# Kernel tuning notes

Hardware: AMD Instinct MI355X
Metric: run time of the kernel (lower is better)

The kernel has to match this reference:

```python
import jax, jax.numpy as jnp
import numpy as np

D_MODEL = 1024
NHEAD = 16
HEAD_DIM = D_MODEL // NHEAD
EPS = 1e-8


def setup_inputs() -> dict:
    key = jax.random.key(0)
    ks = jax.random.split(key, 10)
    B, T = 2, 2048
    s = 1.0 / np.sqrt(D_MODEL)
    return {
        "query": jax.random.normal(ks[0], (B, T, D_MODEL), jnp.float32),
        "key": jax.random.normal(ks[1], (B, T, D_MODEL), jnp.float32),
        "value": jax.random.normal(ks[2], (B, T, D_MODEL), jnp.float32),
        "frac": jax.random.uniform(ks[3], (B, T), jnp.float32),
        "Wq": jax.random.normal(ks[4], (D_MODEL, D_MODEL), jnp.float32) * s,
        "bq": jnp.zeros((D_MODEL,), jnp.float32),
        "Wk": jax.random.normal(ks[5], (D_MODEL, D_MODEL), jnp.float32) * s,
        "bk": jnp.zeros((D_MODEL,), jnp.float32),
        "Wv": jax.random.normal(ks[6], (D_MODEL, D_MODEL), jnp.float32) * s,
        "bv": jnp.zeros((D_MODEL,), jnp.float32),
        "attn_bias": jax.random.normal(ks[7], (HEAD_DIM,), jnp.float32) * 0.02,
        "Wo": jax.random.normal(ks[8], (D_MODEL, D_MODEL), jnp.float32) * s,
        "bo": jnpp if False else jnp.zeros((D_MODEL,), jnp.float32),
    }


def reference(query, key, value, frac, Wq, bq, Wk, bk, Wv, bv, attn_bias, Wo, bo):
    B, T, _ = query.shape
    H, Dh = NHEAD, HEAD_DIM
    scale = Dh ** -0.5

    # torch Linear: x @ W.T + b
    Q = (query @ Wq.T + bq).reshape(B, T, H, Dh).transpose(0, 2, 1, 3)  # [B,H,T,Dh]
    K = (key @ Wk.T + bk).reshape(B, T, H, Dh).transpose(0, 2, 1, 3)
    V = (value @ Wv.T + bv).reshape(B, T, H, Dh).transpose(0, 2, 1, 3)

    # factor_ij = (frac_j - frac_i) / (frac_i*frac_j + eps), shape [B,T,T]
    fi = frac[:, :, None]
    fj = frac[:, None, :]
    factor = (fj - fi) / (fi * fj + EPS)

    # sum_d (Q_i*K_j + attn_bias*factor)_d == QK^T + sum(attn_bias)*factor
    bias_sum = jnp.sum(attn_bias)
    logits = jnp.einsum('bhid,bhjd->bhij', Q, K) + bias_sum * factor[:, None, :, :]
    logits = logits * scale

    probs = jax.nn.softmax(logits, axis=-1)  # dropout p=0.0 (eval)
    out = jnp.einsum('bhij,bhjd->bhid', probs, V)  # [B,H,T,Dh]
    out = out.transpose(0, 2, 1, 3).reshape(B, T, H * Dh)
    return out @ Wo.T + bo
```

## Files before the change

kernel.cpp:

```cpp
#include <hip/hip_runtime.h>

typedef short s16x8 __attribute__((ext_vector_type(8)));
typedef float f32x4 __attribute__((ext_vector_type(4)));
typedef unsigned int u32x2 __attribute__((ext_vector_type(2)));
typedef unsigned short u16;
typedef unsigned int u32;

#define D_MODEL 1024
#define NHEAD   16
#define HD      64
#define TSEQ    2048
#define NB      2
#define MROWS   4096

#define LOG2E 1.4426950408889634f
#define QSCALE (0.125f * LOG2E)

__device__ __forceinline__ u16 f2bf(float f) {
  unsigned u = __builtin_bit_cast(unsigned, f);
  u += 0x7fffu + ((u >> 16) & 1u);
  return (u16)(u >> 16);
}

__device__ __forceinline__ u32 cvtpk(float lo, float hi) {
  u32 r;
  asm("v_cvt_pk_bf16_f32 %0, %1, %2" : "=v"(r) : "v"(lo), "v"(hi));
  return r;
}

__device__ __forceinline__ float exp2fast(float x) {
#if __has_builtin(__builtin_amdgcn_exp2f)
  return __builtin_amdgcn_exp2f(x);
#else
  return exp2f(x);
#endif
}

__device__ __forceinline__ float rcpfast(float x) {
#if __has_builtin(__builtin_amdgcn_rcpf)
  return __builtin_amdgcn_rcpf(x);
#else
  return 1.f / x;
#endif
}

__device__ __forceinline__ void gload16(const void* g, void* l) {
  __builtin_amdgcn_global_load_lds((const __attribute__((address_space(1))) void*)g,
                                   (__attribute__((address_space(3))) void*)l,
                                   16, 0, 0);
}

__global__ void cvt_all(const float* __restrict__ q, const float* __restrict__ k,
                        const float* __restrict__ v, const float* __restrict__ wq,
                        const float* __restrict__ wk, const float* __restrict__ wv,
                        const float* __restrict__ wo, const float* __restrict__ ab,
                        u16* qb, u16* kb, u16* vb, u16* wqb, u16* wkb, u16* wvb, u16* wob,
                        float* bsum) {
  if (blockIdx.x == 16384) {
    if (threadIdx.x < 64) {
      float s = ab[threadIdx.x];
#pragma unroll
      for (int m = 32; m >= 1; m >>= 1) s += __shfl_xor(s, m);
      if (threadIdx.x == 0) bsum[0] = s * 0.125f * LOG2E;
    }
    return;
  }
  int i = blockIdx.x * 256 + threadIdx.x;
  const float* src; u16* dst; int off;
  if (i < 3 * 1048576) {
    int t = i >> 20; off = i & 1048575;
    src = (t == 0) ? q : (t == 1) ? k : v;
    dst = (t == 0) ? qb : (t == 1) ? kb : vb;
  } else {
    int j = i - 3 * 1048576;
    int t = j >> 18; off = j & 262143;
    src = (t == 0) ? wq : (t == 1) ? wk : (t == 2) ? wv : wo;
    dst = (t == 0) ? wqb : (t == 1) ? wkb : (t == 2) ? wvb : wob;
  }
  float4 x = ((const float4*)src)[off];
  ushort4 o;
  o.x = f2bf(x.x); o.y = f2bf(x.y); o.z = f2bf(x.z); o.w = f2bf(x.w);
  ((ushort4*)dst)[off] = o;
}

template <int BM, int BN, int WN>
__device__ __forceinline__ void gemm_core(const u16* __restrict__ A, const u16* __restrict__ Bt,
                                          const float* __restrict__ bias, void* __restrict__ out,
                                          float oscale, int mode, u16* lds) {
  constexpr int K = 1024, N = 1024;
  constexpr int WM = 4 / WN;
  constexpr int WTM = BM / WM, WTN = BN / WN;
  constexpr int MR = WTM / 16, NR = WTN / 16;
  constexpr int ASZ = BM * 32, BSZ = BN * 32;
  constexpr int AISS = ASZ / 2048, BISS = BSZ / 2048;
  u16* lA = lds;
  u16* lB = lds + 2 * ASZ;

  const int tid = threadIdx.x;
  const int wid = tid >> 6, lane = tid & 63;
  const int l15 = lane & 15, lgp = lane >> 4;
  const int wr = wid / WN, wc = wid % WN;
  const int m0 = blockIdx.y * BM, n0 = blockIdx.x * BN;

  const u16* gA[AISS];
  const u16* gB[BISS];
#pragma unroll
  for (int i = 0; i < AISS; ++i) {
    int tp = i * 256 + tid, row = tp % BM, kc = tp / BM;
    gA[i] = A + (size_t)(m0 + row) * K + kc * 8;
  }
#pragma unroll
  for (int i = 0; i < BISS; ++i) {
    int tp = i * 256 + tid, row = tp % BN, kc = tp / BN;
    gB[i] = Bt + (size_t)(n0 + row) * K + kc * 8;
  }

  f32x4 acc[MR][NR];
#pragma unroll
  for (int m = 0; m < MR; ++m)
#pragma unroll
    for (int n = 0; n < NR; ++n) acc[m][n] = (f32x4){0.f, 0.f, 0.f, 0.f};

  auto stage = [&](int buf, int k0) {
#pragma unroll
    for (int i = 0; i < AISS; ++i)
      gload16(gA[i] + k0, lA + buf * ASZ + (i * 256 + tid) * 8);
#pragma unroll
    for (int i = 0; i < BISS; ++i)
      gload16(gB[i] + k0, lB + buf * BSZ + (i * 256 + tid) * 8);
  };

  int cur = 0;
  stage(0, 0);
  __syncthreads();
  for (int k0 = 0; k0 < K; k0 += 32) {
    if (k0 + 32 < K) stage(cur ^ 1, k0 + 32);
    const u16* a = lA + cur * ASZ;
    const u16* b = lB + cur * BSZ;
    s16x8 af[MR], bf[NR];
#pragma unroll
    for (int m = 0; m < MR; ++m)
      af[m] = *(const s16x8*)(a + lgp * BM * 8 + (wr * WTM + m * 16 + l15) * 8);
#pragma unroll
    for (int n = 0; n < NR; ++n)
      bf[n] = *(const s16x8*)(b + lgp * BN * 8 + (wc * WTN + n * 16 + l15) * 8);
    __builtin_amdgcn_s_setprio(1);
#pragma unroll
    for (int m = 0; m < MR; ++m)
#pragma unroll
      for (int n = 0; n < NR; ++n)
        acc[m][n] = __builtin_amdgcn_mfma_f32_16x16x32_bf16(af[m], bf[n], acc[m][n], 0, 0, 0);
    __builtin_amdgcn_s_setprio(0);
    __syncthreads();
    cur ^= 1;
  }

  float bvv[NR];
#pragma unroll
  for (int n = 0; n < NR; ++n) bvv[n] = bias[n0 + wc * WTN + n * 16 + l15];

#pragma unroll
  for (int m = 0; m < MR; ++m) {
    int rowb = m0 + wr * WTM + m * 16 + lgp * 4;
#pragma unroll
    for (int n = 0; n < NR; ++n) {
      int col = n0 + wc * WTN + n * 16 + l15;
#pragma unroll
      for (int r = 0; r < 4; ++r) {
        int row = rowb + r;
        float vv = (acc[m][n][r] + bvv[n]) * oscale;
        if (mode == 2) {
          ((float*)out)[(size_t)row * N + col] = vv;
        } else {
          int b = row >> 11, t = row & 2047;
          int h = col >> 6, d = col & 63;
          u16 x = f2bf(vv);
          if (mode == 0)
            ((u16*)out)[(((size_t)(b * NHEAD + h) * TSEQ + t) << 6) + d] = x;
          else
            ((u16*)out)[(((size_t)(b * NHEAD + h) * HD + d) << 11) + t] = x;
        }
      }
    }
  }
}

__global__ __launch_bounds__(256) void gemm_qkv(const u16* __restrict__ qb, const u16* __restrict__ kb,
                                                const u16* __restrict__ vb,
                                                const u16* __restrict__ Wqb, const u16* __restrict__ Wkb,
                                                const u16* __restrict__ Wvb,
                                                const float* __restrict__ bq, const float* __restrict__ bk,
                                                const float* __restrict__ bv,
                                                u16* Qp, u16* Kp, u16* Vtp) {
  __shared__ __align__(16) u16 lds[2 * 128 * 32 * 2];
  int z = blockIdx.z;
  const u16* A  = (z == 0) ? qb : (z == 1) ? kb : vb;
  const u16* Bt = (z == 0) ? Wqb : (z == 1) ? Wkb : Wvb;
  const float* bias = (z == 0) ? bq : (z == 1) ? bk : bv;
  u16* out = (z == 0) ? Qp : (z == 1) ? Kp : Vtp;
  int mode = (z == 2) ? 1 : 0;
  float oscale = (z == 0) ? QSCALE : 1.0f;
  gemm_core<128, 128, 2>(A, Bt, bias, out, oscale, mode, lds);
}

__global__ __launch_bounds__(256) void gemm_out(const u16* __restrict__ A, const u16* __restrict__ Bt,
                                                const float* __restrict__ bias, float* __restrict__ out) {
  __shared__ __align__(16) u16 lds[2 * 64 * 32 + 2 * 128 * 32];
  gemm_core<64, 128, 4>(A, Bt, bias, out, 1.0f, 2, lds);
}

__global__ __launch_bounds__(256, 4) void attn_kernel(const u16* __restrict__ Qp,
                                                      const u16* __restrict__ Kp,
                                                      const u16* __restrict__ Vt,
                                                      const float* __restrict__ frac,
                                                      const float* __restrict__ bsum,
                                                      u16* __restrict__ aout) {
  __shared__ __align__(16) u16 kbuf[2][64 * 64];
  __shared__ __align__(16) u16 vbuf[2][64 * 64];
  __shared__ __align__(16) u16 plds[4][16 * 64];
  const int tid = threadIdx.x, wid = tid >> 6, lane = tid & 63;
  const int l15 = lane & 15, lgp = lane >> 4;
  const int bh = blockIdx.y, b = bh >> 4, h = bh & 15;
  const u16* Qh = Qp + (size_t)bh * TSEQ * HD;
  const u16* Kh = Kp + (size_t)bh * TSEQ * HD;
  const u16* Vh = Vt + (size_t)bh * HD * TSEQ;
  const float* fb = frac + b * TSEQ;
  const float bs = bsum[0];
  const float THR2 = 24.0f;
  const int q0 = blockIdx.x * 64 + wid * 16;

  const int srow = lane >> 3;
  const int sg8 = ((lane & 7) ^ srow) * 8;
  const int rbase = wid * 8 + srow;

  const int ofs0 = l15 * 64 + ((lgp ^ (l15 & 7)) * 8);
  const int ofs1 = l15 * 64 + (((4 + lgp) ^ (l15 & 7)) * 8);

  s16x8 qf[2];
#pragma unroll
  for (int ks = 0; ks < 2; ++ks)
    qf[ks] = *(const s16x8*)(Qh + (size_t)(q0 + l15) * HD + ks * 32 + lgp * 8);

  const float fi = fb[q0 + l15];
  const float nbfi = -bs * fi;
  float m2run = -1e30f;
  float lsum = 0.f;
  f32x4 o[4];
#pragma unroll
  for (int nd = 0; nd < 4; ++nd) o[nd] = (f32x4){0.f, 0.f, 0.f, 0.f};

  auto stage = [&](int buf, int t) {
    int kv0s = t * 64;
#pragma unroll
    for (int i = 0; i < 2; ++i) {
      int row = i * 32 + rbase;
      gload16(Kh + (size_t)(kv0s + row) * HD + sg8, &kbuf[buf][i * 2048 + wid * 512]);
      gload16(Vh + (size_t)row * TSEQ + kv0s + sg8, &vbuf[buf][i * 2048 + wid * 512]);
    }
  };

  int cur = 0;
  stage(0, 0);
  __syncthreads();

  for (int t = 0; t < TSEQ / 64; ++t) {
    const bool more = (t + 1 < TSEQ / 64);
    if (more) stage(cur ^ 1, t + 1);

    float4 fj4[4];
#pragma unroll
    for (int n = 0; n < 4; ++n)
      fj4[n] = *(const float4*)(fb + t * 64 + n * 16 + lgp * 4);

    const u16* kb = &kbuf[cur][0];
    const u16* vb = &vbuf[cur][0];

    f32x4 s[4];
    __builtin_amdgcn_s_setprio(1);
#pragma unroll
    for (int n = 0; n < 4; ++n) {
      s16x8 kf0 = *(const s16x8*)(kb + n * 1024 + ofs0);
      s16x8 kf1 = *(const s16x8*)(kb + n * 1024 + ofs1);
      f32x4 a = (f32x4){0.f, 0.f, 0.f, 0.f};
      a = __builtin_amdgcn_mfma_f32_16x16x32_bf16(kf0, qf[0], a, 0, 0, 0);
      a = __builtin_amdgcn_mfma_f32_16x16x32_bf16(kf1, qf[1], a, 0, 0, 0);
      s[n] = a;
    }
    __builtin_amdgcn_s_setprio(0);

    float pmax = -1e30f;
#pragma unroll
    for (int n = 0; n < 4; ++n) {
#pragma unroll
      for (int r = 0; r < 4; ++r) {
        float fj = (r == 0) ? fj4[n].x : (r == 1) ? fj4[n].y : (r == 2) ? fj4[n].z : fj4[n].w;
        float num = __builtin_fmaf(bs, fj, nbfi);
        float den = __builtin_fmaf(fi, fj, 1e-8f);
        float l2 = __builtin_fmaf(num, rcpfast(den), s[n][r]);
        s[n][r] = l2;
        pmax = fmaxf(pmax, l2);
      }
    }

    if (__any((pmax - m2run) > THR2)) {
      float tm = fmaxf(pmax, __shfl_xor(pmax, 16));
      tm = fmaxf(tm, __shfl_xor(tm, 32));
      float m2n = fmaxf(m2run, tm);
      float alpha = exp2fast(m2run - m2n);
      lsum *= alpha;
      m2run = m2n;
      float af[4];
#pragma unroll
      for (int r = 0; r < 4; ++r) af[r] = __shfl(alpha, lgp * 4 + r);
#pragma unroll
      for (int nd = 0; nd < 4; ++nd)
#pragma unroll
        for (int r = 0; r < 4; ++r) o[nd][r] *= af[r];
    }

    u32 w[4][2];
    {
      float ps = 0.f;
#pragma unroll
      for (int n = 0; n < 4; ++n) {
#pragma unroll
        for (int s2 = 0; s2 < 2; ++s2) {
          float p0 = exp2fast(s[n][2 * s2 + 0] - m2run);
          float p1 = exp2fast(s[n][2 * s2 + 1] - m2run);
          ps += p0 + p1;
          w[n][s2] = cvtpk(p0, p1);
        }
      }
      lsum += ps;
    }

    u16* pw = &plds[wid][0];
#pragma unroll
    for (int n = 0; n < 4; ++n) {
      int idx = l15 * 64 + ((n * 16 + lgp * 4) ^ ((l15 & 7) << 3));
      *(u32x2*)(pw + idx) = (u32x2){w[n][0], w[n][1]};
    }
    s16x8 pf[2];
#pragma unroll
    for (int ks = 0; ks < 2; ++ks) {
      int idx = l15 * 64 + ((ks * 32 + lgp * 8) ^ ((l15 & 7) << 3));
      pf[ks] = *(const s16x8*)(pw + idx);
    }

    __builtin_amdgcn_s_setprio(1);
#pragma unroll
    for (int nd = 0; nd < 4; ++nd) {
      s16x8 vf0 = *(const s16x8*)(vb + nd * 1024 + ofs0);
      s16x8 vf1 = *(const s16x8*)(vb + nd * 1024 + ofs1);
      o[nd] = __builtin_amdgcn_mfma_f32_16x16x32_bf16(pf[0], vf0, o[nd], 0, 0, 0);
      o[nd] = __builtin_amdgcn_mfma_f32_16x16x32_bf16(pf[1], vf1, o[nd], 0, 0, 0);
    }
    __builtin_amdgcn_s_setprio(0);

    __syncthreads();
    cur ^= 1;
  }

  {
    float l = lsum;
    l += __shfl_xor(l, 16);
    l += __shfl_xor(l, 32);
    float rl[4];
#pragma unroll
    for (int r = 0; r < 4; ++r) rl[r] = __fdividef(1.f, __shfl(l, lgp * 4 + r));
#pragma unroll
    for (int nd = 0; nd < 4; ++nd)
#pragma unroll
      for (int r = 0; r < 4; ++r) {
        int q = q0 + lgp * 4 + r;
        aout[((size_t)(b * TSEQ + q)) * D_MODEL + h * HD + nd * 16 + l15] = f2bf(o[nd][r] * rl[r]);
      }
  }
}

extern "C" void kernel_launch(void* const* d_in, const int* in_sizes, int n_in,
                              void* d_out, int out_size, void* d_ws, size_t ws_size,
                              hipStream_t stream) {
  const float* query = (const float*)d_in[0];
  const float* key_  = (const float*)d_in[1];
  const float* value = (const float*)d_in[2];
  const float* frac  = (const float*)d_in[3];
  const float* Wq    = (const float*)d_in[4];
  const float* bq    = (const float*)d_in[5];
  const float* Wk    = (const float*)d_in[6];
  const float* bk    = (const float*)d_in[7];
  const float* Wv    = (const float*)d_in[8];
  const float* bv    = (const float*)d_in[9];
  const float* abias = (const float*)d_in[10];
  const float* Wo    = (const float*)d_in[11];
  const float* bo    = (const float*)d_in[12];

  char* ws = (char*)d_ws;
  size_t off = 0;
  auto alloc = [&](size_t bytes) { char* p = ws + off; off += (bytes + 255) & ~255ULL; return p; };
  const size_t XB = (size_t)MROWS * D_MODEL * 2;
  const size_t WB = (size_t)D_MODEL * D_MODEL * 2;
  u16* qb  = (u16*)alloc(XB);
  u16* kb  = (u16*)alloc(XB);
  u16* vb  = (u16*)alloc(XB);
  u16* Wqb = (u16*)alloc(WB);
  u16* Wkb = (u16*)alloc(WB);
  u16* Wvb = (u16*)alloc(WB);
  u16* Wob = (u16*)alloc(WB);
  float* bsum = (float*)alloc(256);
  u16* Qp  = (u16*)alloc(XB);
  u16* Kp  = (u16*)alloc(XB);
  u16* Vtp = (u16*)alloc(XB);
  u16* AO  = (u16*)alloc(XB);

  cvt_all<<<dim3(16385), dim3(256), 0, stream>>>(query, key_, value, Wq, Wk, Wv, Wo, abias,
                                                 qb, kb, vb, Wqb, Wkb, Wvb, Wob, bsum);

  gemm_qkv<<<dim3(D_MODEL / 128, MROWS / 128, 3), dim3(256), 0, stream>>>(
      qb, kb, vb, Wqb, Wkb, Wvb, bq, bk, bv, Qp, Kp, Vtp);

  attn_kernel<<<dim3(TSEQ / 64, NB * NHEAD), dim3(256), 0, stream>>>(Qp, Kp, Vtp, frac, bsum, AO);

  gemm_out<<<dim3(D_MODEL / 128, MROWS / 64), dim3(256), 0, stream>>>(AO, Wob, bo, (float*)d_out);
}
```

Before: 184.8 us.

## Split attention KV range in two with a combine kernel

The attention kernel now splits the key/value sequence into two halves along a new grid z dimension. Each half writes an unnormalized bf16 partial output plus its running max and sum, and a new combine kernel merges the halves with rescaling. This doubles the number of attention blocks to fill the GPU better. K tiles are now single-buffered and loaded into registers before a barrier, after which the next tile is prefetched. The cost is an extra launch, extra traffic for the partial outputs, and bf16 rounding of the unnormalized partials. Partials reuse the qb/kb/vb workspace buffers, which are dead after the QKV GEMM.

```diff
diff --git a/kernel.cpp b/kernel.cpp
--- a/kernel.cpp
+++ b/kernel.cpp
@@ -12,6 +12,8 @@
 #define TSEQ    2048
 #define NB      2
 #define MROWS   4096
+#define NSPLIT  2
+#define NTILES  (TSEQ / 64 / NSPLIT)
 
 #define LOG2E 1.4426950408889634f
 #define QSCALE (0.125f * LOG2E)
@@ -20,6 +22,10 @@
   unsigned u = __builtin_bit_cast(unsigned, f);
   u += 0x7fffu + ((u >> 16) & 1u);
   return (u16)(u >> 16);
+}
+
+__device__ __forceinline__ float bf2f(u16 x) {
+  return __builtin_bit_cast(float, (u32)x << 16);
 }
 
 __device__ __forceinline__ u32 cvtpk(float lo, float hi) {
@@ -214,13 +220,19 @@
                                                       const u16* __restrict__ Vt,
                                                       const float* __restrict__ frac,
                                                       const float* __restrict__ bsum,
-                                                      u16* __restrict__ aout) {
-  __shared__ __align__(16) u16 kbuf[2][64 * 64];
+                                                      u16* __restrict__ o0,
+                                                      u16* __restrict__ o1,
+                                                      float2* __restrict__ ml) {
+  __shared__ __align__(16) u16 kbuf[64 * 64];
   __shared__ __align__(16) u16 vbuf[2][64 * 64];
   __shared__ __align__(16) u16 plds[4][16 * 64];
   const int tid = threadIdx.x, wid = tid >> 6, lane = tid & 63;
   const int l15 = lane & 15, lgp = lane >> 4;
   const int bh = blockIdx.y, b = bh >> 4, h = bh & 15;
+  const int z = blockIdx.z;
+  const int kvbase = z * (TSEQ / NSPLIT);
+  u16* opart = z ? o1 : o0;
+  float2* mlz = ml + z * (NB * NHEAD * TSEQ);
   const u16* Qh = Qp + (size_t)bh * TSEQ * HD;
   const u16* Kh = Kp + (size_t)bh * TSEQ * HD;
   const u16* Vh = Vt + (size_t)bh * HD * TSEQ;
@@ -249,41 +261,46 @@
 #pragma unroll
   for (int nd = 0; nd < 4; ++nd) o[nd] = (f32x4){0.f, 0.f, 0.f, 0.f};
 
-  auto stage = [&](int buf, int t) {
-    int kv0s = t * 64;
-#pragma unroll
-    for (int i = 0; i < 2; ++i) {
-      int row = i * 32 + rbase;
-      gload16(Kh + (size_t)(kv0s + row) * HD + sg8, &kbuf[buf][i * 2048 + wid * 512]);
-      gload16(Vh + (size_t)row * TSEQ + kv0s + sg8, &vbuf[buf][i * 2048 + wid * 512]);
-    }
+  auto stageK = [&](int t) {
+    int kv0s = kvbase + t * 64;
+#pragma unroll
+    for (int i = 0; i < 2; ++i)
+      gload16(Kh + (size_t)(kv0s + i * 32 + rbase) * HD + sg8, &kbuf[i * 2048 + wid * 512]);
   };
+  auto stageV = [&](int buf, int t) {
+    int kv0s = kvbase + t * 64;
+#pragma unroll
+    for (int i = 0; i < 2; ++i)
+      gload16(Vh + (size_t)(i * 32 + rbase) * TSEQ + kv0s + sg8, &vbuf[buf][i * 2048 + wid * 512]);
+  };
 
   int cur = 0;
-  stage(0, 0);
+  stageK(0);
+  stageV(0, 0);
   __syncthreads();
 
-  for (int t = 0; t < TSEQ / 64; ++t) {
-    const bool more = (t + 1 < TSEQ / 64);
-    if (more) stage(cur ^ 1, t + 1);
-
+  for (int t = 0; t < NTILES; ++t) {
+    s16x8 kf[4][2];
+#pragma unroll
+    for (int n = 0; n < 4; ++n) {
+      kf[n][0] = *(const s16x8*)(&kbuf[0] + n * 1024 + ofs0);
+      kf[n][1] = *(const s16x8*)(&kbuf[0] + n * 1024 + ofs1);
+    }
     float4 fj4[4];
 #pragma unroll
     for (int n = 0; n < 4; ++n)
-      fj4[n] = *(const float4*)(fb + t * 64 + n * 16 + lgp * 4);
-
-    const u16* kb = &kbuf[cur][0];
-    const u16* vb = &vbuf[cur][0];
+      fj4[n] = *(const float4*)(fb + kvbase + t * 64 + n * 16 + lgp * 4);
+
+    __syncthreads();
+    if (t + 1 < NTILES) { stageK(t + 1); stageV(cur ^ 1, t + 1); }
 
     f32x4 s[4];
     __builtin_amdgcn_s_setprio(1);
 #pragma unroll
     for (int n = 0; n < 4; ++n) {
-      s16x8 kf0 = *(const s16x8*)(kb + n * 1024 + ofs0);
-      s16x8 kf1 = *(const s16x8*)(kb + n * 1024 + ofs1);
       f32x4 a = (f32x4){0.f, 0.f, 0.f, 0.f};
-      a = __builtin_amdgcn_mfma_f32_16x16x32_bf16(kf0, qf[0], a, 0, 0, 0);
-      a = __builtin_amdgcn_mfma_f32_16x16x32_bf16(kf1, qf[1], a, 0, 0, 0);
+      a = __builtin_amdgcn_mfma_f32_16x16x32_bf16(kf[n][0], qf[0], a, 0, 0, 0);
+      a = __builtin_amdgcn_mfma_f32_16x16x32_bf16(kf[n][1], qf[1], a, 0, 0, 0);
       s[n] = a;
     }
     __builtin_amdgcn_s_setprio(0);
@@ -347,11 +364,12 @@
       pf[ks] = *(const s16x8*)(pw + idx);
     }
 
+    const u16* vbp = &vbuf[cur][0];
     __builtin_amdgcn_s_setprio(1);
 #pragma unroll
     for (int nd = 0; nd < 4; ++nd) {
-      s16x8 vf0 = *(const s16x8*)(vb + nd * 1024 + ofs0);
-      s16x8 vf1 = *(const s16x8*)(vb + nd * 1024 + ofs1);
+      s16x8 vf0 = *(const s16x8*)(vbp + nd * 1024 + ofs0);
+      s16x8 vf1 = *(const s16x8*)(vbp + nd * 1024 + ofs1);
       o[nd] = __builtin_amdgcn_mfma_f32_16x16x32_bf16(pf[0], vf0, o[nd], 0, 0, 0);
       o[nd] = __builtin_amdgcn_mfma_f32_16x16x32_bf16(pf[1], vf1, o[nd], 0, 0, 0);
     }
@@ -365,17 +383,42 @@
     float l = lsum;
     l += __shfl_xor(l, 16);
     l += __shfl_xor(l, 32);
-    float rl[4];
-#pragma unroll
-    for (int r = 0; r < 4; ++r) rl[r] = __fdividef(1.f, __shfl(l, lgp * 4 + r));
+    if (lgp == 0)
+      mlz[(bh << 11) + q0 + l15] = make_float2(m2run, l);
 #pragma unroll
     for (int nd = 0; nd < 4; ++nd)
 #pragma unroll
       for (int r = 0; r < 4; ++r) {
         int q = q0 + lgp * 4 + r;
-        aout[((size_t)(b * TSEQ + q)) * D_MODEL + h * HD + nd * 16 + l15] = f2bf(o[nd][r] * rl[r]);
+        opart[((size_t)(b * TSEQ + q)) * D_MODEL + h * HD + nd * 16 + l15] = f2bf(o[nd][r]);
       }
   }
+}
+
+__global__ __launch_bounds__(256) void attn_combine(const u16* __restrict__ o0,
+                                                    const u16* __restrict__ o1,
+                                                    const float2* __restrict__ ml,
+                                                    u16* __restrict__ aout) {
+  int g = blockIdx.x * 256 + threadIdx.x;
+  int bth = g >> 3, j0 = (g & 7) * 8;
+  int b = bth >> 15, t = (bth >> 4) & 2047, h = bth & 15;
+  int mlidx = (((b << 4) | h) << 11) | t;
+  float2 v0 = ml[mlidx];
+  float2 v1 = ml[NB * NHEAD * TSEQ + mlidx];
+  float M = fmaxf(v0.x, v1.x);
+  float a0 = exp2fast(v0.x - M), a1 = exp2fast(v1.x - M);
+  float rd = __fdividef(1.f, __builtin_fmaf(v0.y, a0, v1.y * a1));
+  float s0 = a0 * rd, s1 = a1 * rd;
+  size_t base = (size_t)bth * 64 + j0;
+  s16x8 x0 = *(const s16x8*)(o0 + base);
+  s16x8 x1 = *(const s16x8*)(o1 + base);
+  s16x8 out;
+#pragma unroll
+  for (int j = 0; j < 8; ++j) {
+    float f = __builtin_fmaf(bf2f((u16)x0[j]), s0, bf2f((u16)x1[j]) * s1);
+    out[j] = (short)f2bf(f);
+  }
+  *(s16x8*)(aout + base) = out;
 }
 
 extern "C" void kernel_launch(void* const* d_in, const int* in_sizes, int n_in,
@@ -413,13 +456,20 @@
   u16* Vtp = (u16*)alloc(XB);
   u16* AO  = (u16*)alloc(XB);
 
+  u16* o0 = qb;
+  u16* o1 = kb;
+  float2* ml = (float2*)vb;
+
   cvt_all<<<dim3(16385), dim3(256), 0, stream>>>(query, key_, value, Wq, Wk, Wv, Wo, abias,
                                                  qb, kb, vb, Wqb, Wkb, Wvb, Wob, bsum);
 
   gemm_qkv<<<dim3(D_MODEL / 128, MROWS / 128, 3), dim3(256), 0, stream>>>(
       qb, kb, vb, Wqb, Wkb, Wvb, bq, bk, bv, Qp, Kp, Vtp);
 
-  attn_kernel<<<dim3(TSEQ / 64, NB * NHEAD), dim3(256), 0, stream>>>(Qp, Kp, Vtp, frac, bsum, AO);
+  attn_kernel<<<dim3(TSEQ / 64, NB * NHEAD, NSPLIT), dim3(256), 0, stream>>>(
+      Qp, Kp, Vtp, frac, bsum, o0, o1, ml);
+
+  attn_combine<<<dim3(MROWS * D_MODEL / 8 / 256), dim3(256), 0, stream>>>(o0, o1, ml, AO);
 
   gemm_out<<<dim3(D_MODEL / 128, MROWS / 64), dim3(256), 0, stream>>>(AO, Wob, bo, (float*)d_out);
 }
```

New measurement: 187.4 us. About the same (+1.4%).
